# Optimization experiments

Hardware: AMD Instinct MI355X
Metric: run time of the kernel (lower is better)

The kernel has to match this reference:

```python
import jax, jax.numpy as jnp
import numpy as np

D_MODEL = 2048
N_HEADS = 16
D_K = D_MODEL // N_HEADS
B = 2
S = 2048


def setup_inputs() -> dict:
    key = jax.random.key(0)
    ks = jax.random.split(key, 6)
    scale = 1.0 / np.sqrt(D_MODEL)
    return {
        "inp": jax.random.normal(ks[0], (B, S, D_MODEL), dtype=jnp.float32),
        "wq": jax.random.normal(ks[1], (D_MODEL, D_MODEL), dtype=jnp.float32) * scale,
        "wk": jax.random.normal(ks[2], (D_MODEL, D_MODEL), dtype=jnp.float32) * scale,
        "wv": jax.random.normal(ks[3], (D_MODEL, D_MODEL), dtype=jnp.float32) * scale,
        "wo": jax.random.normal(ks[4], (D_MODEL, D_MODEL), dtype=jnp.float32) * scale,
        "attn_bias": jax.random.normal(ks[5], (1, 1, S, S), dtype=jnp.float32),
        "softcap": 30,
    }


def reference(inp, wq, wk, wv, wo, attn_bias, softcap):
    # inp: [B, S, D]; weights stored torch-style [out, in] -> x @ W^T
    b, s, _ = inp.shape

    def split_heads(x):  # [B,S,D] -> [B,H,S,dk]
        return x.reshape(b, s, N_HEADS, D_K).transpose(0, 2, 1, 3)

    q = split_heads(inp @ wq.T)
    k = split_heads(inp @ wk.T)
    v = split_heads(inp @ wv.T)

    scale = 1.0 / np.sqrt(D_K).astype(np.float32)
    scores = jnp.einsum("bhqd,bhkd->bhqk", q, k) * scale + attn_bias
    cap = jnp.float32(softcap)
    scores = jnp.tanh(scores / cap) * cap  # softcap > 0 branch
    weights = jax.nn.softmax(scores, axis=-1)
    o = jnp.einsum("bhqk,bhkd->bhqd", weights, v)
    o = o.transpose(0, 2, 1, 3).reshape(b, s, D_MODEL)
    return o @ wo.T
```

## Files before the change

### kernel.cpp

```cpp
#include <hip/hip_runtime.h>

#define D_MODEL 2048
#define S_LEN 2048
#define NB 2
#define NH 16
#define DK 128

typedef __attribute__((ext_vector_type(8))) __bf16 bf16x8;
typedef __attribute__((ext_vector_type(4))) float f32x4;
typedef __attribute__((ext_vector_type(2))) float f32x2;

__device__ __forceinline__ unsigned short f2bf(float f) {
    union { __bf16 b; unsigned short u; } cv;
    cv.b = (__bf16)f;
    return cv.u;
}

__device__ __forceinline__ f32x2 pk_fma(f32x2 a, f32x2 b, f32x2 c) {
    f32x2 d;
    asm("v_pk_fma_f32 %0, %1, %2, %3" : "=v"(d) : "v"(a), "v"(b), "v"(c));
    return d;
}
__device__ __forceinline__ f32x2 pk_mul(f32x2 a, f32x2 b) {
    f32x2 d;
    asm("v_pk_mul_f32 %0, %1, %2" : "=v"(d) : "v"(a), "v"(b));
    return d;
}

__device__ __forceinline__ void gld_lds16(const void* g, void* l) {
    __builtin_amdgcn_global_load_lds(
        (const __attribute__((address_space(1))) unsigned int*)g,
        (__attribute__((address_space(3))) unsigned int*)l, 16, 0, 0);
}

__global__ void cast_all_f32_to_bf16(const float* __restrict__ x0, const float* __restrict__ x1,
                                     const float* __restrict__ x2, const float* __restrict__ x3,
                                     const float* __restrict__ x4,
                                     unsigned short* y0, unsigned short* y1,
                                     unsigned short* y2, unsigned short* y3,
                                     unsigned short* y4, int n0, int nw) {
    const int sel = blockIdx.y;
    const float* x = (sel == 0) ? x0 : (sel == 1) ? x1 : (sel == 2) ? x2 : (sel == 3) ? x3 : x4;
    unsigned short* y = (sel == 0) ? y0 : (sel == 1) ? y1 : (sel == 2) ? y2 : (sel == 3) ? y3 : y4;
    const int n4 = (sel == 0) ? n0 : nw;
    int i = blockIdx.x * blockDim.x + threadIdx.x;
    int stride = gridDim.x * blockDim.x;
    const float4* x4p = (const float4*)x;
    ushort4* y4p = (ushort4*)y;
    for (; i < n4; i += stride) {
        float4 v = x4p[i];
        ushort4 o;
        o.x = f2bf(v.x); o.y = f2bf(v.y); o.z = f2bf(v.z); o.w = f2bf(v.w);
        y4p[i] = o;
    }
}

#define BM 128
#define BN 128
#define BK 64

__device__ __forceinline__ void cstore(float* p, float v) { *p = v; }
__device__ __forceinline__ void cstore(unsigned short* p, float v) { *p = f2bf(v); }

template <typename OutT>
__device__ __forceinline__ void gemm_body(const unsigned short* __restrict__ A,
                                          const unsigned short* __restrict__ Bt,
                                          OutT* __restrict__ C,
                                          int M, int N, int K, int m0, int n0) {
    __shared__ __align__(16) unsigned short As[BM * BK];
    __shared__ __align__(16) unsigned short Bs[BN * BK];
    const int tid = threadIdx.x;
    const int lane = tid & 63;
    const int wave = tid >> 6;
    const int quad = lane >> 4;
    const int l15 = lane & 15;
    const int wr = (wave >> 1) * 64;
    const int wc = (wave & 1) * 64;

    const int slotbase = wave * 64 + lane;

    f32x4 zero = {0.f, 0.f, 0.f, 0.f};
    f32x4 acc[4][4];
    for (int i = 0; i < 4; i++)
        for (int j = 0; j < 4; j++) acc[i][j] = zero;

    for (int k0 = 0; k0 < K; k0 += BK) {
        __syncthreads();
#pragma unroll
        for (int t = 0; t < 4; t++) {
            int slot = t * 256 + slotbase;
            int row = slot >> 3;
            int cg = (slot & 7) ^ (row & 7);
            gld_lds16(A + (size_t)(m0 + row) * K + k0 + cg * 8, &As[slot * 8]);
            gld_lds16(Bt + (size_t)(n0 + row) * K + k0 + cg * 8, &Bs[slot * 8]);
        }
        __syncthreads();

        bf16x8 af[4][2], bfr[4][2];
#pragma unroll
        for (int t = 0; t < 4; t++)
#pragma unroll
            for (int c = 0; c < 2; c++) {
                int ch = (c * 4 + quad) ^ (l15 & 7);
                af[t][c]  = *(const bf16x8*)(&As[((wr + t * 16 + l15) * 8 + ch) * 8]);
                bfr[t][c] = *(const bf16x8*)(&Bs[((wc + t * 16 + l15) * 8 + ch) * 8]);
            }
#pragma unroll
        for (int c = 0; c < 2; c++)
#pragma unroll
            for (int mt = 0; mt < 4; mt++)
#pragma unroll
                for (int nt = 0; nt < 4; nt++)
                    acc[mt][nt] = __builtin_amdgcn_mfma_f32_16x16x32_bf16(
                        af[mt][c], bfr[nt][c], acc[mt][nt], 0, 0, 0);
    }

#pragma unroll
    for (int mt = 0; mt < 4; mt++)
#pragma unroll
        for (int nt = 0; nt < 4; nt++)
#pragma unroll
            for (int r = 0; r < 4; r++) {
                int m = m0 + wr + mt * 16 + quad * 4 + r;
                int n = n0 + wc + nt * 16 + l15;
                cstore(&C[(size_t)m * N + n], acc[mt][nt][r]);
            }
}

template <typename OutT>
__global__ __launch_bounds__(256) void gemm_bt(const unsigned short* __restrict__ A,
                                               const unsigned short* __restrict__ Bt,
                                               OutT* __restrict__ C,
                                               int M, int N, int K) {
    gemm_body(A, Bt, C, M, N, K, blockIdx.x * BM, blockIdx.y * BN);
}

__global__ __launch_bounds__(256) void gemm_qkv(const unsigned short* __restrict__ X,
                                                const unsigned short* __restrict__ Wq,
                                                const unsigned short* __restrict__ Wk,
                                                const unsigned short* __restrict__ Wv,
                                                unsigned short* __restrict__ Qo,
                                                unsigned short* __restrict__ Ko,
                                                unsigned short* __restrict__ Vto) {
    const int y = blockIdx.y;
    const unsigned short *A, *Bt;
    unsigned short* C;
    int M, N, m0, n0;
    if (y < 32) {
        const int sel = y >> 4;
        A = X;
        Bt = sel ? Wk : Wq;
        C = sel ? Ko : Qo;
        M = NB * S_LEN; N = D_MODEL;
        m0 = blockIdx.x * BM;
        n0 = (y & 15) * BN;
    } else {
        A = Wv; Bt = X; C = Vto;
        M = D_MODEL; N = NB * S_LEN;
        m0 = (y - 32) * BM;
        n0 = blockIdx.x * BN;
    }
    gemm_body(A, Bt, C, M, N, D_MODEL, m0, n0);
}

#define QT 128
#define PS_STRIDE 72
#define NT (S_LEN / 64)

__global__ __launch_bounds__(512, 4) void flash_attn(
        const unsigned short* __restrict__ Q,
        const unsigned short* __restrict__ K,
        const unsigned short* __restrict__ Vt,
        const float* __restrict__ bias,
        const int* __restrict__ softcap,
        unsigned short* __restrict__ O) {
    __shared__ __align__(16) unsigned short Ks[64 * DK];
    __shared__ __align__(16) unsigned short Vts[2][DK * 64];
    __shared__ __align__(16) unsigned short Ps[8 * 16 * PS_STRIDE];

    const int tid = threadIdx.x;
    const int lane = tid & 63;
    const int wave = tid >> 6;
    const int quad = lane >> 4;
    const int l15 = lane & 15;
    const int q0 = blockIdx.x * QT;
    const int h = blockIdx.y;
    const int b = blockIdx.z;

    const float scale = 0.08838834764831845f;
    const float cap = (float)softcap[0];
    const float LOG2E = 1.4426950408889634f;
    const float kz1 = scale / cap;
    const float kz2 = 1.0f / cap;
    const float KK = cap * LOG2E;

    const f32x2 kz1v = {kz1, kz1};
    const f32x2 kz2v = {kz2, kz2};
    const f32x2 KKv  = {KK, KK};
    const f32x2 mKKv = {-KK, -KK};
    const f32x2 c7v  = {-0.05396825397f, -0.05396825397f};
    const f32x2 c5v  = {0.13333333333f, 0.13333333333f};
    const f32x2 c3v  = {-0.33333333333f, -0.33333333333f};
    const f32x2 onev = {1.0f, 1.0f};

    const size_t head_off = (size_t)b * S_LEN * D_MODEL + (size_t)h * DK;
    const size_t vt_row = (size_t)NB * S_LEN;
    const unsigned short* Vh = Vt + (size_t)h * DK * vt_row + (size_t)b * S_LEN;

    bf16x8 qf[4];
    {
        const unsigned short* Qp = Q + head_off + (size_t)(q0 + wave * 16 + l15) * D_MODEL;
#pragma unroll
        for (int c = 0; c < 4; c++)
            qf[c] = *(const bf16x8*)(Qp + c * 32 + quad * 8);
    }

    f32x4 zero = {0.f, 0.f, 0.f, 0.f};
    float l_part[4] = {0.f, 0.f, 0.f, 0.f};
    f32x4 o_acc[8];
#pragma unroll
    for (int d = 0; d < 8; d++) o_acc[d] = zero;

    unsigned short* Psw = &Ps[wave * 16 * PS_STRIDE];
    const int qrow = q0 + wave * 16 + quad * 4;

    auto stageK = [&](int kbase) {
#pragma unroll
        for (int t = 0; t < 2; t++) {
            int slot = t * 512 + tid;
            int kr = slot >> 4;
            int kc = (slot & 15) ^ (kr & 15);
            gld_lds16(K + head_off + (size_t)(kbase + kr) * D_MODEL + kc * 8,
                      &Ks[slot * 8]);
        }
    };
    auto stageV = [&](int kbase, int buf) {
#pragma unroll
        for (int t = 0; t < 2; t++) {
            int slot = t * 512 + tid;
            int vr = slot >> 3;
            int vc = (slot & 7) ^ (vr & 7);
            gld_lds16(Vh + (size_t)vr * vt_row + kbase + vc * 8,
                      &Vts[buf][slot * 8]);
        }
    };

    stageK(0);
    stageV(0, 0);

    for (int kt = 0; kt < NT; kt++) {
        const int kbase = kt * 64;
        __syncthreads();

        f32x2 bb2[4][2];
#pragma unroll
        for (int nt = 0; nt < 4; nt++) {
            const float* bp = bias + (size_t)qrow * S_LEN + kbase + nt * 16 + l15;
            f32x2 lo, hi;
            lo.x = bp[0];
            lo.y = bp[(size_t)S_LEN];
            hi.x = bp[(size_t)2 * S_LEN];
            hi.y = bp[(size_t)3 * S_LEN];
            bb2[nt][0] = lo;
            bb2[nt][1] = hi;
        }
        __builtin_amdgcn_sched_barrier(0);

        f32x4 s[4];
#pragma unroll
        for (int nt = 0; nt < 4; nt++) s[nt] = zero;
        __builtin_amdgcn_s_setprio(1);
#pragma unroll
        for (int c = 0; c < 4; c++) {
            bf16x8 kf[4];
#pragma unroll
            for (int nt = 0; nt < 4; nt++)
                kf[nt] = *(const bf16x8*)(&Ks[((nt * 16 + l15) * 16 +
                                               ((c * 4 + quad) ^ l15)) * 8]);
#pragma unroll
            for (int nt = 0; nt < 4; nt++)
                s[nt] = __builtin_amdgcn_mfma_f32_16x16x32_bf16(qf[c], kf[nt], s[nt], 0, 0, 0);
        }
        __builtin_amdgcn_s_setprio(0);

        __syncthreads();

        if (kt + 1 < NT) {
            stageK(kbase + 64);
            stageV(kbase + 64, (kt + 1) & 1);
        }

#pragma unroll
        for (int nt = 0; nt < 4; nt++) {
            {
                f32x2 sv = __builtin_shufflevector(s[nt], s[nt], 0, 1);
                f32x2 z = pk_fma(sv, kz1v, pk_mul(bb2[nt][0], kz2v));
                f32x2 z2 = pk_mul(z, z);
                f32x2 w = pk_fma(z2, c7v, c5v);
                w = pk_fma(z2, w, c3v);
                w = pk_fma(z2, w, onev);
                f32x2 t = pk_mul(z, w);
                f32x2 arg = pk_fma(t, KKv, mKKv);
                float p0 = __builtin_amdgcn_exp2f(arg.x);
                float p1 = __builtin_amdgcn_exp2f(arg.y);
                s[nt][0] = p0; s[nt][1] = p1;
                l_part[0] += p0; l_part[1] += p1;
            }
            {
                f32x2 sv = __builtin_shufflevector(s[nt], s[nt], 2, 3);
                f32x2 z = pk_fma(sv, kz1v, pk_mul(bb2[nt][1], kz2v));
                f32x2 z2 = pk_mul(z, z);
                f32x2 w = pk_fma(z2, c7v, c5v);
                w = pk_fma(z2, w, c3v);
                w = pk_fma(z2, w, onev);
                f32x2 t = pk_mul(z, w);
                f32x2 arg = pk_fma(t, KKv, mKKv);
                float p2 = __builtin_amdgcn_exp2f(arg.x);
                float p3 = __builtin_amdgcn_exp2f(arg.y);
                s[nt][2] = p2; s[nt][3] = p3;
                l_part[2] += p2; l_part[3] += p3;
            }
        }

#pragma unroll
        for (int nt = 0; nt < 4; nt++)
#pragma unroll
            for (int r = 0; r < 4; r++)
                Psw[(quad * 4 + r) * PS_STRIDE + nt * 16 + l15] = f2bf(s[nt][r]);

        const unsigned short* Vcur = Vts[kt & 1];
        __builtin_amdgcn_s_setprio(1);
#pragma unroll
        for (int c = 0; c < 2; c++) {
            bf16x8 pf = *(const bf16x8*)(&Psw[l15 * PS_STRIDE + c * 32 + quad * 8]);
#pragma unroll
            for (int dt = 0; dt < 8; dt++) {
                bf16x8 vf = *(const bf16x8*)(&Vcur[((dt * 16 + l15) * 8 +
                                                    ((c * 4 + quad) ^ (l15 & 7))) * 8]);
                o_acc[dt] = __builtin_amdgcn_mfma_f32_16x16x32_bf16(pf, vf, o_acc[dt], 0, 0, 0);
            }
        }
        __builtin_amdgcn_s_setprio(0);
    }

#pragma unroll
    for (int r = 0; r < 4; r++) {
        float l = l_part[r];
        l += __shfl_xor(l, 1, 64);
        l += __shfl_xor(l, 2, 64);
        l += __shfl_xor(l, 4, 64);
        l += __shfl_xor(l, 8, 64);
        float inv = 1.0f / l;
        int row = qrow + r;
        unsigned short* Op = O + (size_t)(b * S_LEN + row) * D_MODEL + h * DK;
#pragma unroll
        for (int dt = 0; dt < 8; dt++)
            Op[dt * 16 + l15] = f2bf(o_acc[dt][r] * inv);
    }
}

extern "C" void kernel_launch(void* const* d_in, const int* in_sizes, int n_in,
                              void* d_out, int out_size, void* d_ws, size_t ws_size,
                              hipStream_t stream) {
    const float* inp = (const float*)d_in[0];
    const float* wq  = (const float*)d_in[1];
    const float* wk  = (const float*)d_in[2];
    const float* wv  = (const float*)d_in[3];
    const float* wo  = (const float*)d_in[4];
    const float* bias = (const float*)d_in[5];
    const int* softcap = (const int*)d_in[6];
    float* out = (float*)d_out;

    unsigned short* ws = (unsigned short*)d_ws;
    const size_t n_inp = (size_t)NB * S_LEN * D_MODEL;
    const size_t n_w = (size_t)D_MODEL * D_MODEL;
    unsigned short* inp_b = ws;
    unsigned short* wq_b = inp_b + n_inp;
    unsigned short* wk_b = wq_b + n_w;
    unsigned short* wv_b = wk_b + n_w;
    unsigned short* wo_b = wv_b + n_w;
    unsigned short* Qb = wo_b + n_w;
    unsigned short* Kb = Qb + n_inp;
    unsigned short* Vtb = Kb + n_inp;
    unsigned short* Ob = Vtb + n_inp;

    cast_all_f32_to_bf16<<<dim3(512, 5), dim3(256), 0, stream>>>(
        inp, wq, wk, wv, wo, inp_b, wq_b, wk_b, wv_b, wo_b,
        (int)(n_inp / 4), (int)(n_w / 4));

    gemm_qkv<<<dim3(NB * S_LEN / BM, 48), 256, 0, stream>>>(
        inp_b, wq_b, wk_b, wv_b, Qb, Kb, Vtb);

    flash_attn<<<dim3(S_LEN / QT, NH, NB), 512, 0, stream>>>(Qb, Kb, Vtb, bias, softcap, Ob);

    dim3 gg(NB * S_LEN / BM, D_MODEL / BN);
    gemm_bt<float><<<gg, 256, 0, stream>>>(Ob, wo_b, out, NB * S_LEN, D_MODEL, D_MODEL);
}
```

Baseline: 420.8 us.

## Software-pipeline GEMM with 4-stage LDS ring and move bias loads after QK

```diff
diff --git a/kernel.cpp b/kernel.cpp
--- a/kernel.cpp
+++ b/kernel.cpp
@@ -57,7 +57,6 @@
 
 #define BM 128
 #define BN 128
-#define BK 64
 
 __device__ __forceinline__ void cstore(float* p, float v) { *p = v; }
 __device__ __forceinline__ void cstore(unsigned short* p, float v) { *p = f2bf(v); }
@@ -66,9 +65,8 @@
 __device__ __forceinline__ void gemm_body(const unsigned short* __restrict__ A,
                                           const unsigned short* __restrict__ Bt,
                                           OutT* __restrict__ C,
-                                          int M, int N, int K, int m0, int n0) {
-    __shared__ __align__(16) unsigned short As[BM * BK];
-    __shared__ __align__(16) unsigned short Bs[BN * BK];
+                                          int M, int N, int m0, int n0) {
+    __shared__ __align__(16) unsigned short lds[4 * 8192];
     const int tid = threadIdx.x;
     const int lane = tid & 63;
     const int wave = tid >> 6;
@@ -77,43 +75,69 @@
     const int wr = (wave >> 1) * 64;
     const int wc = (wave & 1) * 64;
 
-    const int slotbase = wave * 64 + lane;
-
     f32x4 zero = {0.f, 0.f, 0.f, 0.f};
     f32x4 acc[4][4];
     for (int i = 0; i < 4; i++)
         for (int j = 0; j < 4; j++) acc[i][j] = zero;
 
-    for (int k0 = 0; k0 < K; k0 += BK) {
-        __syncthreads();
-#pragma unroll
-        for (int t = 0; t < 4; t++) {
-            int slot = t * 256 + slotbase;
-            int row = slot >> 3;
-            int cg = (slot & 7) ^ (row & 7);
-            gld_lds16(A + (size_t)(m0 + row) * K + k0 + cg * 8, &As[slot * 8]);
-            gld_lds16(Bt + (size_t)(n0 + row) * K + k0 + cg * 8, &Bs[slot * 8]);
-        }
-        __syncthreads();
-
-        bf16x8 af[4][2], bfr[4][2];
-#pragma unroll
-        for (int t = 0; t < 4; t++)
-#pragma unroll
-            for (int c = 0; c < 2; c++) {
-                int ch = (c * 4 + quad) ^ (l15 & 7);
-                af[t][c]  = *(const bf16x8*)(&As[((wr + t * 16 + l15) * 8 + ch) * 8]);
-                bfr[t][c] = *(const bf16x8*)(&Bs[((wc + t * 16 + l15) * 8 + ch) * 8]);
-            }
-#pragma unroll
-        for (int c = 0; c < 2; c++)
-#pragma unroll
-            for (int mt = 0; mt < 4; mt++)
-#pragma unroll
-                for (int nt = 0; nt < 4; nt++)
-                    acc[mt][nt] = __builtin_amdgcn_mfma_f32_16x16x32_bf16(
-                        af[mt][c], bfr[nt][c], acc[mt][nt], 0, 0, 0);
-    }
+    auto stage = [&](int s) {
+        const int kof = s * 32;
+        unsigned short* base = &lds[(s & 3) * 8192];
+#pragma unroll
+        for (int j = 0; j < 2; j++) {
+            int sl = j * 256 + tid;
+            int row = sl >> 2;
+            int c = (sl & 3) ^ ((row >> 1) & 3);
+            gld_lds16(A + (size_t)(m0 + row) * 2048 + kof + c * 8, base + sl * 8);
+            gld_lds16(Bt + (size_t)(n0 + row) * 2048 + kof + c * 8, base + 4096 + sl * 8);
+        }
+    };
+
+    auto compute = [&](int t) {
+        const unsigned short* Ab = &lds[(t & 3) * 8192];
+        const unsigned short* Bb = Ab + 4096;
+        bf16x8 af[4], bfr[4];
+#pragma unroll
+        for (int x = 0; x < 4; x++) {
+            int ra = wr + x * 16 + l15;
+            af[x] = *(const bf16x8*)(Ab + ((ra * 4) + (quad ^ ((ra >> 1) & 3))) * 8);
+            int rb = wc + x * 16 + l15;
+            bfr[x] = *(const bf16x8*)(Bb + ((rb * 4) + (quad ^ ((rb >> 1) & 3))) * 8);
+        }
+#pragma unroll
+        for (int mt = 0; mt < 4; mt++)
+#pragma unroll
+            for (int nt = 0; nt < 4; nt++)
+                acc[mt][nt] = __builtin_amdgcn_mfma_f32_16x16x32_bf16(
+                    af[mt], bfr[nt], acc[mt][nt], 0, 0, 0);
+    };
+
+    stage(0); stage(1); stage(2);
+
+#pragma unroll 4
+    for (int t = 0; t < 61; t++) {
+        asm volatile("s_waitcnt vmcnt(8)" ::: "memory");
+        __builtin_amdgcn_sched_barrier(0);
+        __builtin_amdgcn_s_barrier();
+        __builtin_amdgcn_sched_barrier(0);
+        stage(t + 3);
+        compute(t);
+    }
+    asm volatile("s_waitcnt vmcnt(8)" ::: "memory");
+    __builtin_amdgcn_sched_barrier(0);
+    __builtin_amdgcn_s_barrier();
+    __builtin_amdgcn_sched_barrier(0);
+    compute(61);
+    asm volatile("s_waitcnt vmcnt(4)" ::: "memory");
+    __builtin_amdgcn_sched_barrier(0);
+    __builtin_amdgcn_s_barrier();
+    __builtin_amdgcn_sched_barrier(0);
+    compute(62);
+    asm volatile("s_waitcnt vmcnt(0)" ::: "memory");
+    __builtin_amdgcn_sched_barrier(0);
+    __builtin_amdgcn_s_barrier();
+    __builtin_amdgcn_sched_barrier(0);
+    compute(63);
 
 #pragma unroll
     for (int mt = 0; mt < 4; mt++)
@@ -132,7 +156,7 @@
                                                const unsigned short* __restrict__ Bt,
                                                OutT* __restrict__ C,
                                                int M, int N, int K) {
-    gemm_body(A, Bt, C, M, N, K, blockIdx.x * BM, blockIdx.y * BN);
+    gemm_body(A, Bt, C, M, N, blockIdx.x * BM, blockIdx.y * BN);
 }
 
 __global__ __launch_bounds__(256) void gemm_qkv(const unsigned short* __restrict__ X,
@@ -160,7 +184,7 @@
         m0 = (y - 32) * BM;
         n0 = blockIdx.x * BN;
     }
-    gemm_body(A, Bt, C, M, N, D_MODEL, m0, n0);
+    gemm_body(A, Bt, C, M, N, m0, n0);
 }
 
 #define QT 128
@@ -252,6 +276,25 @@
         const int kbase = kt * 64;
         __syncthreads();
 
+        f32x4 s[4];
+#pragma unroll
+        for (int nt = 0; nt < 4; nt++) s[nt] = zero;
+        __builtin_amdgcn_s_setprio(1);
+#pragma unroll
+        for (int c = 0; c < 4; c++) {
+            bf16x8 kf[4];
+#pragma unroll
+            for (int nt = 0; nt < 4; nt++)
+                kf[nt] = *(const bf16x8*)(&Ks[((nt * 16 + l15) * 16 +
+                                               ((c * 4 + quad) ^ l15)) * 8]);
+#pragma unroll
+            for (int nt = 0; nt < 4; nt++)
+                s[nt] = __builtin_amdgcn_mfma_f32_16x16x32_bf16(qf[c], kf[nt], s[nt], 0, 0, 0);
+        }
+        __builtin_amdgcn_s_setprio(0);
+
+        __syncthreads();
+
         f32x2 bb2[4][2];
 #pragma unroll
         for (int nt = 0; nt < 4; nt++) {
@@ -265,25 +308,6 @@
             bb2[nt][1] = hi;
         }
         __builtin_amdgcn_sched_barrier(0);
-
-        f32x4 s[4];
-#pragma unroll
-        for (int nt = 0; nt < 4; nt++) s[nt] = zero;
-        __builtin_amdgcn_s_setprio(1);
-#pragma unroll
-        for (int c = 0; c < 4; c++) {
-            bf16x8 kf[4];
-#pragma unroll
-            for (int nt = 0; nt < 4; nt++)
-                kf[nt] = *(const bf16x8*)(&Ks[((nt * 16 + l15) * 16 +
-                                               ((c * 4 + quad) ^ l15)) * 8]);
-#pragma unroll
-            for (int nt = 0; nt < 4; nt++)
-                s[nt] = __builtin_amdgcn_mfma_f32_16x16x32_bf16(qf[c], kf[nt], s[nt], 0, 0, 0);
-        }
-        __builtin_amdgcn_s_setprio(0);
-
-        __syncthreads();
 
         if (kt + 1 < NT) {
             stageK(kbase + 64);
```

Result: no change. 412.9 us (-1.9%).
